# Performance work log

Hardware: AMD Instinct MI355X
Metric: run time of the kernel (lower is better)

## Reference

```python
import jax, jax.numpy as jnp
import numpy as np
import math

D_MODEL = 1024
N_HEADS = 16
D_K = D_MODEL // N_HEADS
PADDING_IDX = 0
NEG = -1e9


def setup_inputs() -> dict:
    key = jax.random.key(0)
    ks = jax.random.split(key, 10)
    B, S = 2, 2048
    scale = 1.0 / math.sqrt(D_MODEL)
    x = jax.random.normal(ks[0], (B, S, D_MODEL), dtype=jnp.float32)
    token_ids = jax.random.randint(ks[1], (B, S), 0, 32000)
    wq = jax.random.normal(ks[2], (D_MODEL, D_MODEL), dtype=jnp.float32) * scale
    wk = jax.random.normal(ks[3], (D_MODEL, D_MODEL), dtype=jnp.float32) * scale
    wv = jax.random.normal(ks[4], (D_MODEL, D_MODEL), dtype=jnp.float32) * scale
    wo = jax.random.normal(ks[5], (D_MODEL, D_MODEL), dtype=jnp.float32) * scale
    bq = jnp.zeros((D_MODEL,), jnp.float32)
    bk = jnp.zeros((D_MODEL,), jnp.float32)
    bv = jnp.zeros((D_MODEL,), jnp.float32)
    bo = jnp.zeros((D_MODEL,), jnp.float32)
    return {"x": x, "token_ids": token_ids, "wq": wq, "bq": bq, "wk": wk,
            "bk": bk, "wv": wv, "bv": bv, "wo": wo, "bo": bo}


def _split_heads(t, B, S):
    # [B,S,D] -> [B,H,S,d_k]
    return t.reshape(B, S, N_HEADS, D_K).transpose(0, 2, 1, 3)


def reference(x, token_ids, wq, bq, wk, bk, wv, bv, wo, bo):
    B, S, _ = x.shape
    q = _split_heads(x @ wq + bq, B, S)
    k = _split_heads(x @ wk + bk, B, S)
    v = _split_heads(x @ wv + bv, B, S)
    # padding mask on keys: [B,1,1,S]; causal mask: [1,1,S,S]
    pad = (token_ids == PADDING_IDX)[:, None, None, :]
    causal = jnp.triu(jnp.ones((S, S), dtype=bool), k=1)[None, None, :, :]
    mask = pad | causal
    scores = jnp.einsum("bhqd,bhkd->bhqk", q, k) / math.sqrt(D_K)
    scores = jnp.where(mask, NEG, scores)
    attn = jax.nn.softmax(scores, axis=-1)
    out = jnp.einsum("bhqk,bhkd->bhqd", attn, v)
    out = out.transpose(0, 2, 1, 3).reshape(B, S, D_MODEL)
    return out @ wo + bo, attn
```

## Files before the change

### kernel.cpp

```cpp
#include <hip/hip_runtime.h>
#include <hip/hip_bf16.h>
#include <math.h>

#define S_LEN 2048
#define B_SZ 2
#define DMODEL 1024
#define NH 16
#define DK 64
#define QKVN 3072
#define SM_SHIFT 8.0f

typedef __attribute__((ext_vector_type(8))) short bf16x8;
typedef __attribute__((ext_vector_type(4))) float f32x4;

__device__ inline short f2bf(float f) {
    __hip_bfloat16 h = __float2bfloat16(f);
    return __builtin_bit_cast(short, h);
}
__device__ inline float bf2f(short s) {
    unsigned int u = ((unsigned int)(unsigned short)s) << 16;
    return __builtin_bit_cast(float, u);
}
__device__ inline f32x4 mfma16(bf16x8 a, bf16x8 b, f32x4 c) {
    return __builtin_amdgcn_mfma_f32_16x16x32_bf16(a, b, c, 0, 0, 0);
}
__device__ inline void gl_lds16(const void* g, void* l) {
    __builtin_amdgcn_global_load_lds(
        (const __attribute__((address_space(1))) void*)g,
        (__attribute__((address_space(3))) void*)l, 16, 0, 0);
}

__global__ __launch_bounds__(256) void cvt_bf16(const float* __restrict__ in,
                                                short* __restrict__ out, int n4) {
    int i = blockIdx.x * 256 + threadIdx.x;
    if (i < n4) {
        float4 v = *(const float4*)&in[(size_t)i * 4];
        short4 o = { f2bf(v.x), f2bf(v.y), f2bf(v.z), f2bf(v.w) };
        *(short4*)&out[(size_t)i * 4] = o;
    }
}

__global__ __launch_bounds__(256) void wtrans(const float* __restrict__ W,
                                              short* __restrict__ Wt) {
    __shared__ __align__(16) short T[64][72];
    const int k0 = blockIdx.x * 64, n0 = blockIdx.y * 64;
    const int tid = threadIdx.x;
#pragma unroll
    for (int i = 0; i < 4; ++i) {
        int idx = tid + i * 256;
        int kr = idx >> 4, n4 = idx & 15;
        float4 v = *(const float4*)&W[(size_t)(k0 + kr) * DMODEL + n0 + n4 * 4];
        short4 o = { f2bf(v.x), f2bf(v.y), f2bf(v.z), f2bf(v.w) };
        *(short4*)&T[kr][n4 * 4] = o;
    }
    __syncthreads();
#pragma unroll
    for (int i = 0; i < 2; ++i) {
        int idx = tid + i * 256;
        int n = idx >> 3, c8 = idx & 7;
        short v[8];
#pragma unroll
        for (int j = 0; j < 8; ++j) v[j] = T[c8 * 8 + j][n];
        *(int4*)&Wt[(size_t)(n0 + n) * DMODEL + k0 + c8 * 8] = *(int4*)v;
    }
}

__global__ __launch_bounds__(256) void cbias_cat(const float* __restrict__ bq,
                                                 const float* __restrict__ bk,
                                                 const float* __restrict__ bv,
                                                 float* __restrict__ cb) {
    int i = blockIdx.x * 256 + threadIdx.x;
    if (i < QKVN)
        cb[i] = i < 1024 ? bq[i] : (i < 2048 ? bk[i - 1024] : bv[i - 2048]);
}

__global__ __launch_bounds__(256) void gemm_qkv(
    const short* __restrict__ A, const short* __restrict__ Bt,
    const float* __restrict__ bias, short* __restrict__ C,
    int M, int N, int K) {
    __shared__ __align__(16) short As[128][64];
    __shared__ __align__(16) short Bs[128][64];
    const int row0 = blockIdx.y * 128, col0 = blockIdx.x * 128;
    const int tid = threadIdx.x;
    const int w = tid >> 6, l = tid & 63, lm = l & 15, quad = l >> 4;
    const int wm = (w >> 1) * 64, wn = (w & 1) * 64;
    const int lrow = tid >> 3, lc8 = tid & 7;
    f32x4 acc[4][4] = {};

    for (int k0 = 0; k0 < K; k0 += 64) {
        __syncthreads();
#pragma unroll
        for (int i = 0; i < 4; ++i)
            gl_lds16(&A[(size_t)(row0 + i * 32 + lrow) * K + k0 + lc8 * 8],
                     (short*)As + (i * 32 + w * 8) * 64);
#pragma unroll
        for (int i = 0; i < 4; ++i)
            gl_lds16(&Bt[(size_t)(col0 + i * 32 + lrow) * K + k0 + lc8 * 8],
                     (short*)Bs + (i * 32 + w * 8) * 64);
        __syncthreads();
#pragma unroll
        for (int kc = 0; kc < 2; ++kc) {
            bf16x8 a[4], b[4];
#pragma unroll
            for (int mi = 0; mi < 4; ++mi)
                a[mi] = *(const bf16x8*)&As[wm + mi * 16 + lm][kc * 32 + quad * 8];
#pragma unroll
            for (int ni = 0; ni < 4; ++ni)
                b[ni] = *(const bf16x8*)&Bs[wn + ni * 16 + lm][kc * 32 + quad * 8];
#pragma unroll
            for (int mi = 0; mi < 4; ++mi)
#pragma unroll
                for (int ni = 0; ni < 4; ++ni)
                    acc[mi][ni] = mfma16(a[mi], b[ni], acc[mi][ni]);
        }
    }
#pragma unroll
    for (int mi = 0; mi < 4; ++mi)
#pragma unroll
        for (int ni = 0; ni < 4; ++ni) {
            int col = col0 + wn + ni * 16 + lm;
            float bs = bias[col];
#pragma unroll
            for (int r = 0; r < 4; ++r) {
                int row = row0 + wm + mi * 16 + quad * 4 + r;
                C[(size_t)row * N + col] = f2bf(acc[mi][ni][r] + bs);
            }
        }
}

__global__ __launch_bounds__(256) void vtrans(const short* __restrict__ QKV,
                                              short* __restrict__ Vt) {
    __shared__ __align__(16) short T[64][72];
    const int bh = blockIdx.y, b = bh >> 4, h = bh & 15;
    const int s0 = blockIdx.x * 64;
    const int tid = threadIdx.x;
#pragma unroll
    for (int i = 0; i < 2; ++i) {
        int idx = tid + i * 256;
        int r = idx >> 3, c8 = idx & 7;
        *(int4*)&T[r][c8 * 8] =
            *(const int4*)&QKV[((size_t)(b * S_LEN + s0 + r)) * QKVN + 2048 + h * DK + c8 * 8];
    }
    __syncthreads();
#pragma unroll
    for (int i = 0; i < 2; ++i) {
        int idx = tid + i * 256;
        int d = idx >> 3, c8 = idx & 7;
        short v[8];
#pragma unroll
        for (int j = 0; j < 8; ++j) v[j] = T[c8 * 8 + j][d];
        *(int4*)&Vt[((size_t)(bh * DK + d)) * S_LEN + s0 + c8 * 8] = *(int4*)v;
    }
}

__global__ __launch_bounds__(256) void gemm_out(
    const short* __restrict__ A, const short* __restrict__ Bt,
    const float* __restrict__ bias, float* __restrict__ Cout,
    int M, int N, int K) {
    __shared__ __align__(16) short As[64][72];
    __shared__ __align__(16) short Bs[64][72];
    const int row0 = blockIdx.y * 64, col0 = blockIdx.x * 64;
    const int tid = threadIdx.x;
    const int w = tid >> 6, l = tid & 63, lm = l & 15, quad = l >> 4;
    const int wm = (w >> 1) * 32, wn = (w & 1) * 32;
    f32x4 acc[2][2] = {};

    for (int k0 = 0; k0 < K; k0 += 64) {
        __syncthreads();
#pragma unroll
        for (int i = 0; i < 2; ++i) {
            int idx = tid + i * 256;
            int r = idx >> 3, c8 = idx & 7;
            *(int4*)&As[r][c8 * 8] = *(const int4*)&A[(size_t)(row0 + r) * K + k0 + c8 * 8];
            *(int4*)&Bs[r][c8 * 8] = *(const int4*)&Bt[(size_t)(col0 + r) * K + k0 + c8 * 8];
        }
        __syncthreads();
#pragma unroll
        for (int kc = 0; kc < 2; ++kc) {
            bf16x8 a0 = *(const bf16x8*)&As[wm + lm][kc * 32 + quad * 8];
            bf16x8 a1 = *(const bf16x8*)&As[wm + 16 + lm][kc * 32 + quad * 8];
            bf16x8 b0 = *(const bf16x8*)&Bs[wn + lm][kc * 32 + quad * 8];
            bf16x8 b1 = *(const bf16x8*)&Bs[wn + 16 + lm][kc * 32 + quad * 8];
            acc[0][0] = mfma16(a0, b0, acc[0][0]);
            acc[0][1] = mfma16(a0, b1, acc[0][1]);
            acc[1][0] = mfma16(a1, b0, acc[1][0]);
            acc[1][1] = mfma16(a1, b1, acc[1][1]);
        }
    }
#pragma unroll
    for (int mi = 0; mi < 2; ++mi)
#pragma unroll
        for (int ni = 0; ni < 2; ++ni)
#pragma unroll
            for (int r = 0; r < 4; ++r) {
                int row = row0 + wm + mi * 16 + quad * 4 + r;
                int col = col0 + wn + ni * 16 + lm;
                Cout[(size_t)row * N + col] = acc[mi][ni][r] + bias[col];
            }
}

__global__ __launch_bounds__(256) void fnp_scan(const int* __restrict__ tok,
                                                int* __restrict__ fnp) {
    __shared__ int mn;
    const int b = blockIdx.x;
    if (threadIdx.x == 0) mn = S_LEN;
    __syncthreads();
    int loc = S_LEN;
    for (int s = threadIdx.x; s < S_LEN; s += 256)
        if (tok[b * S_LEN + s] != 0) loc = min(loc, s);
    atomicMin(&mn, loc);
    __syncthreads();
    if (threadIdx.x == 0) fnp[b] = mn;
}

__global__ __launch_bounds__(256) void flash_lsum(
    const short* __restrict__ QKV, const int* __restrict__ tok,
    float* __restrict__ Lrow) {
    const int bh = blockIdx.y, b = bh >> 4, h = bh & 15;
    const int qt = blockIdx.x, q0 = qt * 64;
    const int tid = threadIdx.x;
    const int w = tid >> 6, l = tid & 63, lm = l & 15, quad = l >> 4;
    __shared__ __align__(16) short Qs[64][72];
    __shared__ __align__(16) short Ks[64][72];
    __shared__ float padf[64];

#pragma unroll
    for (int i = 0; i < 2; ++i) {
        int idx = tid + i * 256;
        int r = idx >> 3, c8 = idx & 7;
        *(int4*)&Qs[r][c8 * 8] =
            *(const int4*)&QKV[((size_t)(b * S_LEN + q0 + r)) * QKVN + h * DK + c8 * 8];
    }

    float lsum[4] = {0.f, 0.f, 0.f, 0.f};

    for (int kt = 0; kt <= qt; ++kt) {
        __syncthreads();
#pragma unroll
        for (int i = 0; i < 2; ++i) {
            int idx = tid + i * 256;
            int r = idx >> 3, c8 = idx & 7;
            *(int4*)&Ks[r][c8 * 8] =
                *(const int4*)&QKV[((size_t)(b * S_LEN + kt * 64 + r)) * QKVN + 1024 + h * DK + c8 * 8];
        }
        if (tid < 64) padf[tid] = (tok[b * S_LEN + kt * 64 + tid] == 0) ? 1.f : 0.f;
        __syncthreads();

#pragma unroll
        for (int nt = 0; nt < 4; ++nt) {
            f32x4 acc = {0.f, 0.f, 0.f, 0.f};
#pragma unroll
            for (int kc = 0; kc < 2; ++kc) {
                bf16x8 a = *(const bf16x8*)&Qs[w * 16 + lm][kc * 32 + quad * 8];
                bf16x8 bb = *(const bf16x8*)&Ks[nt * 16 + lm][kc * 32 + quad * 8];
                acc = mfma16(a, bb, acc);
            }
            int kcol = kt * 64 + nt * 16 + lm;
            bool pad = padf[nt * 16 + lm] != 0.f;
#pragma unroll
            for (int r = 0; r < 4; ++r) {
                int qrow = q0 + w * 16 + quad * 4 + r;
                bool msk = pad || (kcol > qrow);
                lsum[r] += msk ? 0.f : __expf(acc[r] * 0.125f - SM_SHIFT);
            }
        }
    }

#pragma unroll
    for (int off = 1; off < 16; off <<= 1)
#pragma unroll
        for (int r = 0; r < 4; ++r) lsum[r] += __shfl_xor(lsum[r], off);

    if (lm == 0) {
#pragma unroll
        for (int r = 0; r < 4; ++r)
            Lrow[(size_t)bh * S_LEN + q0 + w * 16 + quad * 4 + r] = lsum[r];
    }
}

__global__ __launch_bounds__(256) void flash_pb(
    const short* __restrict__ QKV, const short* __restrict__ Vt,
    const int* __restrict__ tok, const float* __restrict__ Lrow,
    float* __restrict__ attn, short* __restrict__ ctxb) {
    const int bh = blockIdx.y, b = bh >> 4, h = bh & 15;
    const int qt = blockIdx.x, q0 = qt * 64;
    const int tid = threadIdx.x;
    const int w = tid >> 6, l = tid & 63, lm = l & 15, quad = l >> 4;
    __shared__ __align__(16) short Qs[64][72];
    __shared__ __align__(16) short Ks[64][72];
    __shared__ __align__(16) short Vs[64][72];
    __shared__ __align__(16) short Ps[64][72];
    __shared__ float padf[64];

#pragma unroll
    for (int i = 0; i < 2; ++i) {
        int idx = tid + i * 256;
        int r = idx >> 3, c8 = idx & 7;
        *(int4*)&Qs[r][c8 * 8] =
            *(const int4*)&QKV[((size_t)(b * S_LEN + q0 + r)) * QKVN + h * DK + c8 * 8];
    }

    float linv[4];
#pragma unroll
    for (int r = 0; r < 4; ++r)
        linv[r] = 1.f / Lrow[(size_t)bh * S_LEN + q0 + w * 16 + quad * 4 + r];

    f32x4 oacc[4] = {};

    for (int kt = 0; kt <= qt; ++kt) {
        __syncthreads();
#pragma unroll
        for (int i = 0; i < 2; ++i) {
            int idx = tid + i * 256;
            int r = idx >> 3, c8 = idx & 7;
            *(int4*)&Ks[r][c8 * 8] =
                *(const int4*)&QKV[((size_t)(b * S_LEN + kt * 64 + r)) * QKVN + 1024 + h * DK + c8 * 8];
            *(int4*)&Vs[r][c8 * 8] =
                *(const int4*)&Vt[((size_t)(bh * DK + r)) * S_LEN + kt * 64 + c8 * 8];
        }
        if (tid < 64) padf[tid] = (tok[b * S_LEN + kt * 64 + tid] == 0) ? 1.f : 0.f;
        __syncthreads();

#pragma unroll
        for (int nt = 0; nt < 4; ++nt) {
            f32x4 acc = {0.f, 0.f, 0.f, 0.f};
#pragma unroll
            for (int kc = 0; kc < 2; ++kc) {
                bf16x8 a = *(const bf16x8*)&Qs[w * 16 + lm][kc * 32 + quad * 8];
                bf16x8 bb = *(const bf16x8*)&Ks[nt * 16 + lm][kc * 32 + quad * 8];
                acc = mfma16(a, bb, acc);
            }
            int kcol = kt * 64 + nt * 16 + lm;
            bool pad = padf[nt * 16 + lm] != 0.f;
#pragma unroll
            for (int r = 0; r < 4; ++r) {
                int qrow = q0 + w * 16 + quad * 4 + r;
                bool msk = pad || (kcol > qrow);
                float p = msk ? 0.f : __expf(acc[r] * 0.125f - SM_SHIFT) * linv[r];
                attn[((size_t)bh * S_LEN + qrow) * S_LEN + kcol] = p;
                Ps[w * 16 + quad * 4 + r][nt * 16 + lm] = f2bf(p);
            }
        }
#pragma unroll
        for (int kc = 0; kc < 2; ++kc) {
            bf16x8 a = *(const bf16x8*)&Ps[w * 16 + lm][kc * 32 + quad * 8];
#pragma unroll
            for (int dt = 0; dt < 4; ++dt) {
                bf16x8 bv = *(const bf16x8*)&Vs[dt * 16 + lm][kc * 32 + quad * 8];
                oacc[dt] = mfma16(a, bv, oacc[dt]);
            }
        }
    }

#pragma unroll
    for (int dt = 0; dt < 4; ++dt)
#pragma unroll
        for (int r = 0; r < 4; ++r) {
            int qrow = q0 + w * 16 + quad * 4 + r;
            ctxb[((size_t)(b * S_LEN + qrow)) * DMODEL + h * DK + dt * 16 + lm] =
                f2bf(oacc[dt][r]);
        }
}

__global__ __launch_bounds__(256) void fill_upper(float* __restrict__ attn) {
    const int qt = blockIdx.x, bh = blockIdx.y;
    const int ce = (qt + 1) * 64;
    const int n = S_LEN - ce;
    if (n <= 0) return;
    const int n4 = n >> 2;
    float4 z = {0.f, 0.f, 0.f, 0.f};
    float* base = attn + ((size_t)bh * S_LEN + qt * 64) * S_LEN;
    for (int i = threadIdx.x; i < 64 * n4; i += 256) {
        int row = i / n4, c = i % n4;
        *(float4*)&base[(size_t)row * S_LEN + ce + c * 4] = z;
    }
}

__global__ __launch_bounds__(256) void fix_fullmask(
    const int* __restrict__ fnp, const short* __restrict__ QKV,
    float* __restrict__ attn, short* __restrict__ ctxb) {
    const int b = blockIdx.x >> 11, q = blockIdx.x & 2047;
    if (q >= fnp[b]) return;
    const float u = 1.f / (float)S_LEN;
    float4 uu = {u, u, u, u};
    for (int i = threadIdx.x; i < NH * (S_LEN / 4); i += 256) {
        int h = i / (S_LEN / 4), c4 = i % (S_LEN / 4);
        *(float4*)&attn[(((size_t)(b * NH + h) * S_LEN + q)) * S_LEN + c4 * 4] = uu;
    }
    for (int d = threadIdx.x; d < DMODEL; d += 256) {
        float sv = 0.f;
        for (int s = 0; s < S_LEN; ++s)
            sv += bf2f(QKV[((size_t)(b * S_LEN + s)) * QKVN + 2048 + d]);
        ctxb[((size_t)(b * S_LEN + q)) * DMODEL + d] = f2bf(sv * u);
    }
}

extern "C" void kernel_launch(void* const* d_in, const int* in_sizes, int n_in,
                              void* d_out, int out_size, void* d_ws, size_t ws_size,
                              hipStream_t stream) {
    const float* x  = (const float*)d_in[0];
    const int*  tok = (const int*)d_in[1];
    const float* wq = (const float*)d_in[2];
    const float* bq = (const float*)d_in[3];
    const float* wk = (const float*)d_in[4];
    const float* bk = (const float*)d_in[5];
    const float* wv = (const float*)d_in[6];
    const float* bv = (const float*)d_in[7];
    const float* wo = (const float*)d_in[8];
    const float* bo = (const float*)d_in[9];

    float* out  = (float*)d_out;
    float* attn = out + (size_t)B_SZ * S_LEN * DMODEL;

    const size_t NTOK = (size_t)B_SZ * S_LEN;
    const size_t NE   = NTOK * DMODEL;
    const size_t WSZ  = (size_t)DMODEL * DMODEL;
    short* xb    = (short*)d_ws;
    short* Wt3   = xb + NE;
    short* Wto   = Wt3 + 3 * WSZ;
    short* QKVb  = Wto + WSZ;
    short* Vt    = QKVb + NTOK * QKVN;
    short* ctxb  = Vt + NE;
    float* cbias = (float*)(ctxb + NE);
    float* Lrow  = cbias + QKVN;
    int*   fnp   = (int*)(Lrow + (size_t)B_SZ * NH * S_LEN);

    dim3 blk(256);

    cvt_bf16<<<dim3((int)(NE / 4 / 256)), blk, 0, stream>>>(x, xb, (int)(NE / 4));
    wtrans<<<dim3(16, 16), blk, 0, stream>>>(wq, Wt3 + 0 * WSZ);
    wtrans<<<dim3(16, 16), blk, 0, stream>>>(wk, Wt3 + 1 * WSZ);
    wtrans<<<dim3(16, 16), blk, 0, stream>>>(wv, Wt3 + 2 * WSZ);
    wtrans<<<dim3(16, 16), blk, 0, stream>>>(wo, Wto);
    cbias_cat<<<dim3(QKVN / 256), blk, 0, stream>>>(bq, bk, bv, cbias);

    gemm_qkv<<<dim3(QKVN / 128, (int)(NTOK / 128)), blk, 0, stream>>>(
        xb, Wt3, cbias, QKVb, (int)NTOK, QKVN, DMODEL);

    vtrans<<<dim3(S_LEN / 64, B_SZ * NH), blk, 0, stream>>>(QKVb, Vt);
    fnp_scan<<<dim3(B_SZ), blk, 0, stream>>>(tok, fnp);

    flash_lsum<<<dim3(S_LEN / 64, B_SZ * NH), blk, 0, stream>>>(QKVb, tok, Lrow);
    flash_pb<<<dim3(S_LEN / 64, B_SZ * NH), blk, 0, stream>>>(QKVb, Vt, tok, Lrow,
                                                              attn, ctxb);
    fill_upper<<<dim3(S_LEN / 64, B_SZ * NH), blk, 0, stream>>>(attn);
    fix_fullmask<<<dim3(B_SZ * S_LEN), blk, 0, stream>>>(fnp, QKVb, attn, ctxb);

    gemm_out<<<dim3(DMODEL / 64, (int)(NTOK / 64)), blk, 0, stream>>>(
        ctxb, Wto, bo, out, (int)NTOK, DMODEL, DMODEL);
}
```

Before: 837.0 us.

## Split attention into per-tile score kernel and separate PV GEMM; reuse 128-tile GEMM

The fused flash_pb kernel, which looped over key tiles and wrote probabilities while computing P·V, is split in two. A new attn_scores kernel launches one block per (q-tile, k-tile) pair, writes the normalized probabilities with coalesced float4 stores staged through shared memory, and zero-fills upper-triangle tiles, which replaces the fill_upper kernel. A separate pv_gemm then re-reads the fp32 attention matrix, converts it to bf16 and multiplies by V. The output projection now uses the templated 128x128 GEMM. The aim is better parallelism and store coalescing in the imbalanced causal kernel, at the cost of re-reading the large attention matrix from memory.

New measurement: 907.0 us. +8.4%, slower.

```diff
diff --git a/kernel.cpp b/kernel.cpp
--- a/kernel.cpp
+++ b/kernel.cpp
@@ -74,9 +74,10 @@
         cb[i] = i < 1024 ? bq[i] : (i < 2048 ? bk[i - 1024] : bv[i - 2048]);
 }
 
-__global__ __launch_bounds__(256) void gemm_qkv(
+template <bool OUT_BF16>
+__global__ __launch_bounds__(256) void gemm128(
     const short* __restrict__ A, const short* __restrict__ Bt,
-    const float* __restrict__ bias, short* __restrict__ C,
+    const float* __restrict__ bias, void* __restrict__ Cout,
     int M, int N, int K) {
     __shared__ __align__(16) short As[128][64];
     __shared__ __align__(16) short Bs[128][64];
@@ -123,7 +124,11 @@
 #pragma unroll
             for (int r = 0; r < 4; ++r) {
                 int row = row0 + wm + mi * 16 + quad * 4 + r;
-                C[(size_t)row * N + col] = f2bf(acc[mi][ni][r] + bs);
+                float v = acc[mi][ni][r] + bs;
+                if (OUT_BF16)
+                    ((short*)Cout)[(size_t)row * N + col] = f2bf(v);
+                else
+                    ((float*)Cout)[(size_t)row * N + col] = v;
             }
         }
 }
@@ -151,52 +156,6 @@
         for (int j = 0; j < 8; ++j) v[j] = T[c8 * 8 + j][d];
         *(int4*)&Vt[((size_t)(bh * DK + d)) * S_LEN + s0 + c8 * 8] = *(int4*)v;
     }
-}
-
-__global__ __launch_bounds__(256) void gemm_out(
-    const short* __restrict__ A, const short* __restrict__ Bt,
-    const float* __restrict__ bias, float* __restrict__ Cout,
-    int M, int N, int K) {
-    __shared__ __align__(16) short As[64][72];
-    __shared__ __align__(16) short Bs[64][72];
-    const int row0 = blockIdx.y * 64, col0 = blockIdx.x * 64;
-    const int tid = threadIdx.x;
-    const int w = tid >> 6, l = tid & 63, lm = l & 15, quad = l >> 4;
-    const int wm = (w >> 1) * 32, wn = (w & 1) * 32;
-    f32x4 acc[2][2] = {};
-
-    for (int k0 = 0; k0 < K; k0 += 64) {
-        __syncthreads();
-#pragma unroll
-        for (int i = 0; i < 2; ++i) {
-            int idx = tid + i * 256;
-            int r = idx >> 3, c8 = idx & 7;
-            *(int4*)&As[r][c8 * 8] = *(const int4*)&A[(size_t)(row0 + r) * K + k0 + c8 * 8];
-            *(int4*)&Bs[r][c8 * 8] = *(const int4*)&Bt[(size_t)(col0 + r) * K + k0 + c8 * 8];
-        }
-        __syncthreads();
-#pragma unroll
-        for (int kc = 0; kc < 2; ++kc) {
-            bf16x8 a0 = *(const bf16x8*)&As[wm + lm][kc * 32 + quad * 8];
-            bf16x8 a1 = *(const bf16x8*)&As[wm + 16 + lm][kc * 32 + quad * 8];
-            bf16x8 b0 = *(const bf16x8*)&Bs[wn + lm][kc * 32 + quad * 8];
-            bf16x8 b1 = *(const bf16x8*)&Bs[wn + 16 + lm][kc * 32 + quad * 8];
-            acc[0][0] = mfma16(a0, b0, acc[0][0]);
-            acc[0][1] = mfma16(a0, b1, acc[0][1]);
-            acc[1][0] = mfma16(a1, b0, acc[1][0]);
-            acc[1][1] = mfma16(a1, b1, acc[1][1]);
-        }
-    }
-#pragma unroll
-    for (int mi = 0; mi < 2; ++mi)
-#pragma unroll
-        for (int ni = 0; ni < 2; ++ni)
-#pragma unroll
-            for (int r = 0; r < 4; ++r) {
-                int row = row0 + wm + mi * 16 + quad * 4 + r;
-                int col = col0 + wn + ni * 16 + lm;
-                Cout[(size_t)row * N + col] = acc[mi][ni][r] + bias[col];
-            }
 }
 
 __global__ __launch_bounds__(256) void fnp_scan(const int* __restrict__ tok,
@@ -278,19 +237,32 @@
     }
 }
 
-__global__ __launch_bounds__(256) void flash_pb(
-    const short* __restrict__ QKV, const short* __restrict__ Vt,
-    const int* __restrict__ tok, const float* __restrict__ Lrow,
-    float* __restrict__ attn, short* __restrict__ ctxb) {
+__global__ __launch_bounds__(256) void attn_scores(
+    const short* __restrict__ QKV, const int* __restrict__ tok,
+    const float* __restrict__ Lrow, float* __restrict__ attn) {
     const int bh = blockIdx.y, b = bh >> 4, h = bh & 15;
-    const int qt = blockIdx.x, q0 = qt * 64;
-    const int tid = threadIdx.x;
+    const int qt = blockIdx.x >> 5, kt = blockIdx.x & 31;
+    const int q0 = qt * 64, k0 = kt * 64;
+    const int tid = threadIdx.x;
+    float* tileb = attn + ((size_t)bh * S_LEN + q0) * S_LEN + k0;
+
+    if (kt > qt) {
+        float4 z = {0.f, 0.f, 0.f, 0.f};
+#pragma unroll
+        for (int i = 0; i < 4; ++i) {
+            int c = tid + i * 256;
+            int row = c >> 4, c4 = c & 15;
+            *(float4*)&tileb[(size_t)row * S_LEN + c4 * 4] = z;
+        }
+        return;
+    }
+
     const int w = tid >> 6, l = tid & 63, lm = l & 15, quad = l >> 4;
     __shared__ __align__(16) short Qs[64][72];
     __shared__ __align__(16) short Ks[64][72];
-    __shared__ __align__(16) short Vs[64][72];
-    __shared__ __align__(16) short Ps[64][72];
+    __shared__ __align__(16) float Ps[64][68];
     __shared__ float padf[64];
+    __shared__ float sinv[64];
 
 #pragma unroll
     for (int i = 0; i < 2; ++i) {
@@ -298,55 +270,79 @@
         int r = idx >> 3, c8 = idx & 7;
         *(int4*)&Qs[r][c8 * 8] =
             *(const int4*)&QKV[((size_t)(b * S_LEN + q0 + r)) * QKVN + h * DK + c8 * 8];
-    }
-
-    float linv[4];
-#pragma unroll
-    for (int r = 0; r < 4; ++r)
-        linv[r] = 1.f / Lrow[(size_t)bh * S_LEN + q0 + w * 16 + quad * 4 + r];
-
+        *(int4*)&Ks[r][c8 * 8] =
+            *(const int4*)&QKV[((size_t)(b * S_LEN + k0 + r)) * QKVN + 1024 + h * DK + c8 * 8];
+    }
+    if (tid < 64) {
+        padf[tid] = (tok[b * S_LEN + k0 + tid] == 0) ? 1.f : 0.f;
+        sinv[tid] = 1.f / Lrow[(size_t)bh * S_LEN + q0 + tid];
+    }
+    __syncthreads();
+
+#pragma unroll
+    for (int nt = 0; nt < 4; ++nt) {
+        f32x4 acc = {0.f, 0.f, 0.f, 0.f};
+#pragma unroll
+        for (int kc = 0; kc < 2; ++kc) {
+            bf16x8 a = *(const bf16x8*)&Qs[w * 16 + lm][kc * 32 + quad * 8];
+            bf16x8 bb = *(const bf16x8*)&Ks[nt * 16 + lm][kc * 32 + quad * 8];
+            acc = mfma16(a, bb, acc);
+        }
+        int kcol = k0 + nt * 16 + lm;
+        bool pad = padf[nt * 16 + lm] != 0.f;
+#pragma unroll
+        for (int r = 0; r < 4; ++r) {
+            int trow = w * 16 + quad * 4 + r;
+            bool msk = pad || (kcol > q0 + trow);
+            Ps[trow][nt * 16 + lm] =
+                msk ? 0.f : __expf(acc[r] * 0.125f - SM_SHIFT) * sinv[trow];
+        }
+    }
+    __syncthreads();
+#pragma unroll
+    for (int i = 0; i < 4; ++i) {
+        int c = tid + i * 256;
+        int row = c >> 4, c4 = c & 15;
+        *(float4*)&tileb[(size_t)row * S_LEN + c4 * 4] = *(const float4*)&Ps[row][c4 * 4];
+    }
+}
+
+__global__ __launch_bounds__(256) void pv_gemm(
+    const float* __restrict__ attn, const short* __restrict__ Vt,
+    short* __restrict__ ctxb) {
+    const int bh = blockIdx.y, b = bh >> 4, h = bh & 15;
+    const int qt = blockIdx.x, q0 = qt * 64;
+    const int tid = threadIdx.x;
+    const int w = tid >> 6, l = tid & 63, lm = l & 15, quad = l >> 4;
+    __shared__ __align__(16) short As[64][72];
+    __shared__ __align__(16) short Bs[64][72];
     f32x4 oacc[4] = {};
 
     for (int kt = 0; kt <= qt; ++kt) {
         __syncthreads();
+#pragma unroll
+        for (int i = 0; i < 4; ++i) {
+            int c = tid + i * 256;
+            int row = c >> 4, c4 = c & 15;
+            float4 v = *(const float4*)&attn[((size_t)bh * S_LEN + q0 + row) * S_LEN +
+                                             kt * 64 + c4 * 4];
+            short4 o = { f2bf(v.x), f2bf(v.y), f2bf(v.z), f2bf(v.w) };
+            *(short4*)&As[row][c4 * 4] = o;
+        }
 #pragma unroll
         for (int i = 0; i < 2; ++i) {
             int idx = tid + i * 256;
             int r = idx >> 3, c8 = idx & 7;
-            *(int4*)&Ks[r][c8 * 8] =
-                *(const int4*)&QKV[((size_t)(b * S_LEN + kt * 64 + r)) * QKVN + 1024 + h * DK + c8 * 8];
-            *(int4*)&Vs[r][c8 * 8] =
+            *(int4*)&Bs[r][c8 * 8] =
                 *(const int4*)&Vt[((size_t)(bh * DK + r)) * S_LEN + kt * 64 + c8 * 8];
         }
-        if (tid < 64) padf[tid] = (tok[b * S_LEN + kt * 64 + tid] == 0) ? 1.f : 0.f;
-        __syncthreads();
-
-#pragma unroll
-        for (int nt = 0; nt < 4; ++nt) {
-            f32x4 acc = {0.f, 0.f, 0.f, 0.f};
-#pragma unroll
-            for (int kc = 0; kc < 2; ++kc) {
-                bf16x8 a = *(const bf16x8*)&Qs[w * 16 + lm][kc * 32 + quad * 8];
-                bf16x8 bb = *(const bf16x8*)&Ks[nt * 16 + lm][kc * 32 + quad * 8];
-                acc = mfma16(a, bb, acc);
-            }
-            int kcol = kt * 64 + nt * 16 + lm;
-            bool pad = padf[nt * 16 + lm] != 0.f;
-#pragma unroll
-            for (int r = 0; r < 4; ++r) {
-                int qrow = q0 + w * 16 + quad * 4 + r;
-                bool msk = pad || (kcol > qrow);
-                float p = msk ? 0.f : __expf(acc[r] * 0.125f - SM_SHIFT) * linv[r];
-                attn[((size_t)bh * S_LEN + qrow) * S_LEN + kcol] = p;
-                Ps[w * 16 + quad * 4 + r][nt * 16 + lm] = f2bf(p);
-            }
-        }
+        __syncthreads();
 #pragma unroll
         for (int kc = 0; kc < 2; ++kc) {
-            bf16x8 a = *(const bf16x8*)&Ps[w * 16 + lm][kc * 32 + quad * 8];
+            bf16x8 a = *(const bf16x8*)&As[w * 16 + lm][kc * 32 + quad * 8];
 #pragma unroll
             for (int dt = 0; dt < 4; ++dt) {
-                bf16x8 bv = *(const bf16x8*)&Vs[dt * 16 + lm][kc * 32 + quad * 8];
+                bf16x8 bv = *(const bf16x8*)&Bs[dt * 16 + lm][kc * 32 + quad * 8];
                 oacc[dt] = mfma16(a, bv, oacc[dt]);
             }
         }
@@ -360,20 +356,6 @@
             ctxb[((size_t)(b * S_LEN + qrow)) * DMODEL + h * DK + dt * 16 + lm] =
                 f2bf(oacc[dt][r]);
         }
-}
-
-__global__ __launch_bounds__(256) void fill_upper(float* __restrict__ attn) {
-    const int qt = blockIdx.x, bh = blockIdx.y;
-    const int ce = (qt + 1) * 64;
-    const int n = S_LEN - ce;
-    if (n <= 0) return;
-    const int n4 = n >> 2;
-    float4 z = {0.f, 0.f, 0.f, 0.f};
-    float* base = attn + ((size_t)bh * S_LEN + qt * 64) * S_LEN;
-    for (int i = threadIdx.x; i < 64 * n4; i += 256) {
-        int row = i / n4, c = i % n4;
-        *(float4*)&base[(size_t)row * S_LEN + ce + c * 4] = z;
-    }
 }
 
 __global__ __launch_bounds__(256) void fix_fullmask(
@@ -434,18 +416,19 @@
     wtrans<<<dim3(16, 16), blk, 0, stream>>>(wo, Wto);
     cbias_cat<<<dim3(QKVN / 256), blk, 0, stream>>>(bq, bk, bv, cbias);
 
-    gemm_qkv<<<dim3(QKVN / 128, (int)(NTOK / 128)), blk, 0, stream>>>(
+    gemm128<true><<<dim3(QKVN / 128, (int)(NTOK / 128)), blk, 0, stream>>>(
         xb, Wt3, cbias, QKVb, (int)NTOK, QKVN, DMODEL);
 
     vtrans<<<dim3(S_LEN / 64, B_SZ * NH), blk, 0, stream>>>(QKVb, Vt);
     fnp_scan<<<dim3(B_SZ), blk, 0, stream>>>(tok, fnp);
 
     flash_lsum<<<dim3(S_LEN / 64, B_SZ * NH), blk, 0, stream>>>(QKVb, tok, Lrow);
-    flash_pb<<<dim3(S_LEN / 64, B_SZ * NH), blk, 0, stream>>>(QKVb, Vt, tok, Lrow,
-                                                              attn, ctxb);
-    fill_upper<<<dim3(S_LEN / 64, B_SZ * NH), blk, 0, stream>>>(attn);
+
+    attn_scores<<<dim3((S_LEN / 64) * (S_LEN / 64), B_SZ * NH), blk, 0, stream>>>(
+        QKVb, tok, Lrow, attn);
+    pv_gemm<<<dim3(S_LEN / 64, B_SZ * NH), blk, 0, stream>>>(attn, Vt, ctxb);
     fix_fullmask<<<dim3(B_SZ * S_LEN), blk, 0, stream>>>(fnp, QKVb, attn, ctxb);
 
-    gemm_out<<<dim3(DMODEL / 64, (int)(NTOK / 64)), blk, 0, stream>>>(
+    gemm128<false><<<dim3(DMODEL / 128, (int)(NTOK / 128)), blk, 0, stream>>>(
         ctxb, Wto, bo, out, (int)NTOK, DMODEL, DMODEL);
 }
```

## Parallelize row-sum pass over query-key tiles and fuse upper-triangle zero fill

Applied to the files above, without the earlier changes.

The row-sum (softmax denominator) pass now launches one block per (query tile, key tile) pair instead of looping serially over key tiles per query tile. Partial sums are combined into a pre-zeroed buffer with atomic adds. Blocks for tiles above the diagonal write zeros to the attention output instead, which replaces the separate fill kernel. This targets the load imbalance and low parallelism of the causal loop, at the cost of more blocks, reloading Q for every tile, and atomic traffic.

Measured after the change: 828.4 us. No clear change (-1.0%).

```diff
diff --git a/kernel.cpp b/kernel.cpp
--- a/kernel.cpp
+++ b/kernel.cpp
@@ -74,7 +74,7 @@
         cb[i] = i < 1024 ? bq[i] : (i < 2048 ? bk[i - 1024] : bv[i - 2048]);
 }
 
-__global__ __launch_bounds__(256) void gemm_qkv(
+__global__ __launch_bounds__(256) void gemm128(
     const short* __restrict__ A, const short* __restrict__ Bt,
     const float* __restrict__ bias, short* __restrict__ C,
     int M, int N, int K) {
@@ -128,32 +128,7 @@
         }
 }
 
-__global__ __launch_bounds__(256) void vtrans(const short* __restrict__ QKV,
-                                              short* __restrict__ Vt) {
-    __shared__ __align__(16) short T[64][72];
-    const int bh = blockIdx.y, b = bh >> 4, h = bh & 15;
-    const int s0 = blockIdx.x * 64;
-    const int tid = threadIdx.x;
-#pragma unroll
-    for (int i = 0; i < 2; ++i) {
-        int idx = tid + i * 256;
-        int r = idx >> 3, c8 = idx & 7;
-        *(int4*)&T[r][c8 * 8] =
-            *(const int4*)&QKV[((size_t)(b * S_LEN + s0 + r)) * QKVN + 2048 + h * DK + c8 * 8];
-    }
-    __syncthreads();
-#pragma unroll
-    for (int i = 0; i < 2; ++i) {
-        int idx = tid + i * 256;
-        int d = idx >> 3, c8 = idx & 7;
-        short v[8];
-#pragma unroll
-        for (int j = 0; j < 8; ++j) v[j] = T[c8 * 8 + j][d];
-        *(int4*)&Vt[((size_t)(bh * DK + d)) * S_LEN + s0 + c8 * 8] = *(int4*)v;
-    }
-}
-
-__global__ __launch_bounds__(256) void gemm_out(
+__global__ __launch_bounds__(256) void gemm64(
     const short* __restrict__ A, const short* __restrict__ Bt,
     const float* __restrict__ bias, float* __restrict__ Cout,
     int M, int N, int K) {
@@ -197,6 +172,31 @@
                 int col = col0 + wn + ni * 16 + lm;
                 Cout[(size_t)row * N + col] = acc[mi][ni][r] + bias[col];
             }
+}
+
+__global__ __launch_bounds__(256) void vtrans(const short* __restrict__ QKV,
+                                              short* __restrict__ Vt) {
+    __shared__ __align__(16) short T[64][72];
+    const int bh = blockIdx.y, b = bh >> 4, h = bh & 15;
+    const int s0 = blockIdx.x * 64;
+    const int tid = threadIdx.x;
+#pragma unroll
+    for (int i = 0; i < 2; ++i) {
+        int idx = tid + i * 256;
+        int r = idx >> 3, c8 = idx & 7;
+        *(int4*)&T[r][c8 * 8] =
+            *(const int4*)&QKV[((size_t)(b * S_LEN + s0 + r)) * QKVN + 2048 + h * DK + c8 * 8];
+    }
+    __syncthreads();
+#pragma unroll
+    for (int i = 0; i < 2; ++i) {
+        int idx = tid + i * 256;
+        int d = idx >> 3, c8 = idx & 7;
+        short v[8];
+#pragma unroll
+        for (int j = 0; j < 8; ++j) v[j] = T[c8 * 8 + j][d];
+        *(int4*)&Vt[((size_t)(bh * DK + d)) * S_LEN + s0 + c8 * 8] = *(int4*)v;
+    }
 }
 
 __global__ __launch_bounds__(256) void fnp_scan(const int* __restrict__ tok,
@@ -213,12 +213,31 @@
     if (threadIdx.x == 0) fnp[b] = mn;
 }
 
-__global__ __launch_bounds__(256) void flash_lsum(
+__global__ __launch_bounds__(256) void lzero(float* __restrict__ L) {
+    float4 z = {0.f, 0.f, 0.f, 0.f};
+    *(float4*)&L[(size_t)(blockIdx.x * 256 + threadIdx.x) * 4] = z;
+}
+
+__global__ __launch_bounds__(256) void lsum_par(
     const short* __restrict__ QKV, const int* __restrict__ tok,
-    float* __restrict__ Lrow) {
+    float* __restrict__ Lrow, float* __restrict__ attn) {
     const int bh = blockIdx.y, b = bh >> 4, h = bh & 15;
-    const int qt = blockIdx.x, q0 = qt * 64;
-    const int tid = threadIdx.x;
+    const int qt = blockIdx.x >> 5, kt = blockIdx.x & 31;
+    const int q0 = qt * 64, k0 = kt * 64;
+    const int tid = threadIdx.x;
+
+    if (kt > qt) {
+        float4 z = {0.f, 0.f, 0.f, 0.f};
+        float* tileb = attn + ((size_t)bh * S_LEN + q0) * S_LEN + k0;
+#pragma unroll
+        for (int i = 0; i < 4; ++i) {
+            int c = tid + i * 256;
+            int row = c >> 4, c4 = c & 15;
+            *(float4*)&tileb[(size_t)row * S_LEN + c4 * 4] = z;
+        }
+        return;
+    }
+
     const int w = tid >> 6, l = tid & 63, lm = l & 15, quad = l >> 4;
     __shared__ __align__(16) short Qs[64][72];
     __shared__ __align__(16) short Ks[64][72];
@@ -230,9 +249,71 @@
         int r = idx >> 3, c8 = idx & 7;
         *(int4*)&Qs[r][c8 * 8] =
             *(const int4*)&QKV[((size_t)(b * S_LEN + q0 + r)) * QKVN + h * DK + c8 * 8];
-    }
-
-    float lsum[4] = {0.f, 0.f, 0.f, 0.f};
+        *(int4*)&Ks[r][c8 * 8] =
+            *(const int4*)&QKV[((size_t)(b * S_LEN + k0 + r)) * QKVN + 1024 + h * DK + c8 * 8];
+    }
+    if (tid < 64) padf[tid] = (tok[b * S_LEN + k0 + tid] == 0) ? 1.f : 0.f;
+    __syncthreads();
+
+    float rp[4] = {0.f, 0.f, 0.f, 0.f};
+#pragma unroll
+    for (int nt = 0; nt < 4; ++nt) {
+        f32x4 acc = {0.f, 0.f, 0.f, 0.f};
+#pragma unroll
+        for (int kc = 0; kc < 2; ++kc) {
+            bf16x8 a = *(const bf16x8*)&Qs[w * 16 + lm][kc * 32 + quad * 8];
+            bf16x8 bb = *(const bf16x8*)&Ks[nt * 16 + lm][kc * 32 + quad * 8];
+            acc = mfma16(a, bb, acc);
+        }
+        int kcol = k0 + nt * 16 + lm;
+        bool pad = padf[nt * 16 + lm] != 0.f;
+#pragma unroll
+        for (int r = 0; r < 4; ++r) {
+            int qrow = q0 + w * 16 + quad * 4 + r;
+            bool msk = pad || (kcol > qrow);
+            rp[r] += msk ? 0.f : __expf(acc[r] * 0.125f - SM_SHIFT);
+        }
+    }
+#pragma unroll
+    for (int off = 1; off < 16; off <<= 1)
+#pragma unroll
+        for (int r = 0; r < 4; ++r) rp[r] += __shfl_xor(rp[r], off);
+
+    if (lm == 0) {
+#pragma unroll
+        for (int r = 0; r < 4; ++r)
+            atomicAdd(&Lrow[(size_t)bh * S_LEN + q0 + w * 16 + quad * 4 + r], rp[r]);
+    }
+}
+
+__global__ __launch_bounds__(256) void flash_pb(
+    const short* __restrict__ QKV, const short* __restrict__ Vt,
+    const int* __restrict__ tok, const float* __restrict__ Lrow,
+    float* __restrict__ attn, short* __restrict__ ctxb) {
+    const int bh = blockIdx.y, b = bh >> 4, h = bh & 15;
+    const int qt = blockIdx.x, q0 = qt * 64;
+    const int tid = threadIdx.x;
+    const int w = tid >> 6, l = tid & 63, lm = l & 15, quad = l >> 4;
+    __shared__ __align__(16) short Qs[64][72];
+    __shared__ __align__(16) short Ks[64][72];
+    __shared__ __align__(16) short Vs[64][72];
+    __shared__ __align__(16) short Ps[64][72];
+    __shared__ float padf[64];
+
+#pragma unroll
+    for (int i = 0; i < 2; ++i) {
+        int idx = tid + i * 256;
+        int r = idx >> 3, c8 = idx & 7;
+        *(int4*)&Qs[r][c8 * 8] =
+            *(const int4*)&QKV[((size_t)(b * S_LEN + q0 + r)) * QKVN + h * DK + c8 * 8];
+    }
+
+    float linv[4];
+#pragma unroll
+    for (int r = 0; r < 4; ++r)
+        linv[r] = 1.f / Lrow[(size_t)bh * S_LEN + q0 + w * 16 + quad * 4 + r];
+
+    f32x4 oacc[4] = {};
 
     for (int kt = 0; kt <= qt; ++kt) {
         __syncthreads();
@@ -242,6 +323,8 @@
             int r = idx >> 3, c8 = idx & 7;
             *(int4*)&Ks[r][c8 * 8] =
                 *(const int4*)&QKV[((size_t)(b * S_LEN + kt * 64 + r)) * QKVN + 1024 + h * DK + c8 * 8];
+            *(int4*)&Vs[r][c8 * 8] =
+                *(const int4*)&Vt[((size_t)(bh * DK + r)) * S_LEN + kt * 64 + c8 * 8];
         }
         if (tid < 64) padf[tid] = (tok[b * S_LEN + kt * 64 + tid] == 0) ? 1.f : 0.f;
         __syncthreads();
@@ -261,81 +344,6 @@
             for (int r = 0; r < 4; ++r) {
                 int qrow = q0 + w * 16 + quad * 4 + r;
                 bool msk = pad || (kcol > qrow);
-                lsum[r] += msk ? 0.f : __expf(acc[r] * 0.125f - SM_SHIFT);
-            }
-        }
-    }
-
-#pragma unroll
-    for (int off = 1; off < 16; off <<= 1)
-#pragma unroll
-        for (int r = 0; r < 4; ++r) lsum[r] += __shfl_xor(lsum[r], off);
-
-    if (lm == 0) {
-#pragma unroll
-        for (int r = 0; r < 4; ++r)
-            Lrow[(size_t)bh * S_LEN + q0 + w * 16 + quad * 4 + r] = lsum[r];
-    }
-}
-
-__global__ __launch_bounds__(256) void flash_pb(
-    const short* __restrict__ QKV, const short* __restrict__ Vt,
-    const int* __restrict__ tok, const float* __restrict__ Lrow,
-    float* __restrict__ attn, short* __restrict__ ctxb) {
-    const int bh = blockIdx.y, b = bh >> 4, h = bh & 15;
-    const int qt = blockIdx.x, q0 = qt * 64;
-    const int tid = threadIdx.x;
-    const int w = tid >> 6, l = tid & 63, lm = l & 15, quad = l >> 4;
-    __shared__ __align__(16) short Qs[64][72];
-    __shared__ __align__(16) short Ks[64][72];
-    __shared__ __align__(16) short Vs[64][72];
-    __shared__ __align__(16) short Ps[64][72];
-    __shared__ float padf[64];
-
-#pragma unroll
-    for (int i = 0; i < 2; ++i) {
-        int idx = tid + i * 256;
-        int r = idx >> 3, c8 = idx & 7;
-        *(int4*)&Qs[r][c8 * 8] =
-            *(const int4*)&QKV[((size_t)(b * S_LEN + q0 + r)) * QKVN + h * DK + c8 * 8];
-    }
-
-    float linv[4];
-#pragma unroll
-    for (int r = 0; r < 4; ++r)
-        linv[r] = 1.f / Lrow[(size_t)bh * S_LEN + q0 + w * 16 + quad * 4 + r];
-
-    f32x4 oacc[4] = {};
-
-    for (int kt = 0; kt <= qt; ++kt) {
-        __syncthreads();
-#pragma unroll
-        for (int i = 0; i < 2; ++i) {
-            int idx = tid + i * 256;
-            int r = idx >> 3, c8 = idx & 7;
-            *(int4*)&Ks[r][c8 * 8] =
-                *(const int4*)&QKV[((size_t)(b * S_LEN + kt * 64 + r)) * QKVN + 1024 + h * DK + c8 * 8];
-            *(int4*)&Vs[r][c8 * 8] =
-                *(const int4*)&Vt[((size_t)(bh * DK + r)) * S_LEN + kt * 64 + c8 * 8];
-        }
-        if (tid < 64) padf[tid] = (tok[b * S_LEN + kt * 64 + tid] == 0) ? 1.f : 0.f;
-        __syncthreads();
-
-#pragma unroll
-        for (int nt = 0; nt < 4; ++nt) {
-            f32x4 acc = {0.f, 0.f, 0.f, 0.f};
-#pragma unroll
-            for (int kc = 0; kc < 2; ++kc) {
-                bf16x8 a = *(const bf16x8*)&Qs[w * 16 + lm][kc * 32 + quad * 8];
-                bf16x8 bb = *(const bf16x8*)&Ks[nt * 16 + lm][kc * 32 + quad * 8];
-                acc = mfma16(a, bb, acc);
-            }
-            int kcol = kt * 64 + nt * 16 + lm;
-            bool pad = padf[nt * 16 + lm] != 0.f;
-#pragma unroll
-            for (int r = 0; r < 4; ++r) {
-                int qrow = q0 + w * 16 + quad * 4 + r;
-                bool msk = pad || (kcol > qrow);
                 float p = msk ? 0.f : __expf(acc[r] * 0.125f - SM_SHIFT) * linv[r];
                 attn[((size_t)bh * S_LEN + qrow) * S_LEN + kcol] = p;
                 Ps[w * 16 + quad * 4 + r][nt * 16 + lm] = f2bf(p);
@@ -360,20 +368,6 @@
             ctxb[((size_t)(b * S_LEN + qrow)) * DMODEL + h * DK + dt * 16 + lm] =
                 f2bf(oacc[dt][r]);
         }
-}
-
-__global__ __launch_bounds__(256) void fill_upper(float* __restrict__ attn) {
-    const int qt = blockIdx.x, bh = blockIdx.y;
-    const int ce = (qt + 1) * 64;
-    const int n = S_LEN - ce;
-    if (n <= 0) return;
-    const int n4 = n >> 2;
-    float4 z = {0.f, 0.f, 0.f, 0.f};
-    float* base = attn + ((size_t)bh * S_LEN + qt * 64) * S_LEN;
-    for (int i = threadIdx.x; i < 64 * n4; i += 256) {
-        int row = i / n4, c = i % n4;
-        *(float4*)&base[(size_t)row * S_LEN + ce + c * 4] = z;
-    }
 }
 
 __global__ __launch_bounds__(256) void fix_fullmask(
@@ -433,19 +427,20 @@
     wtrans<<<dim3(16, 16), blk, 0, stream>>>(wv, Wt3 + 2 * WSZ);
     wtrans<<<dim3(16, 16), blk, 0, stream>>>(wo, Wto);
     cbias_cat<<<dim3(QKVN / 256), blk, 0, stream>>>(bq, bk, bv, cbias);
-
-    gemm_qkv<<<dim3(QKVN / 128, (int)(NTOK / 128)), blk, 0, stream>>>(
+    lzero<<<dim3((int)(B_SZ * NH * S_LEN / 1024)), blk, 0, stream>>>(Lrow);
+
+    gemm128<<<dim3(QKVN / 128, (int)(NTOK / 128)), blk, 0, stream>>>(
         xb, Wt3, cbias, QKVb, (int)NTOK, QKVN, DMODEL);
 
     vtrans<<<dim3(S_LEN / 64, B_SZ * NH), blk, 0, stream>>>(QKVb, Vt);
     fnp_scan<<<dim3(B_SZ), blk, 0, stream>>>(tok, fnp);
 
-    flash_lsum<<<dim3(S_LEN / 64, B_SZ * NH), blk, 0, stream>>>(QKVb, tok, Lrow);
+    lsum_par<<<dim3((S_LEN / 64) * (S_LEN / 64), B_SZ * NH), blk, 0, stream>>>(
+        QKVb, tok, Lrow, attn);
     flash_pb<<<dim3(S_LEN / 64, B_SZ * NH), blk, 0, stream>>>(QKVb, Vt, tok, Lrow,
                                                               attn, ctxb);
-    fill_upper<<<dim3(S_LEN / 64, B_SZ * NH), blk, 0, stream>>>(attn);
     fix_fullmask<<<dim3(B_SZ * S_LEN), blk, 0, stream>>>(fnp, QKVb, attn, ctxb);
 
-    gemm_out<<<dim3(DMODEL / 64, (int)(NTOK / 64)), blk, 0, stream>>>(
+    gemm64<<<dim3(DMODEL / 64, (int)(NTOK / 64)), blk, 0, stream>>>(
         ctxb, Wto, bo, out, (int)NTOK, DMODEL, DMODEL);
 }
```
